# Kernel optimization log

Hardware: AMD Instinct MI355X
Metric: run time of the kernel (lower is better)

## Reference

```python
import jax, jax.numpy as jnp
import numpy as np


def conv1x1(x, w, b):
    # x: [B, Cin, D, H, W], w: [Cout, Cin], b: [Cout]
    return jnp.einsum('bcdhw,oc->bodhw', x, w) + b[None, :, None, None, None]


def setup_inputs() -> dict:
    key = jax.random.key(0)
    ks = jax.random.split(key, 9)
    B, C, D, H, W = 2, 64, 16, 16, 16
    Cc = 64          # context_dim
    C8 = C // 8      # inner attention dim
    s = 0.05
    return {
        'x': jax.random.normal(ks[0], (B, C, D, H, W), jnp.float32),
        'context': jax.random.normal(ks[1], (B, Cc, D, H, W), jnp.float32),
        'Wq': jax.random.normal(ks[2], (C8, C), jnp.float32) * s,
        'bq': jax.random.normal(ks[3], (C8,), jnp.float32) * s,
        'Wk': jax.random.normal(ks[4], (C8, Cc), jnp.float32) * s,
        'bk': jax.random.normal(ks[5], (C8,), jnp.float32) * s,
        'Wv': jax.random.normal(ks[6], (C, Cc), jnp.float32) * s,
        'bv': jax.random.normal(ks[7], (C,), jnp.float32) * s,
        'gamma': jax.random.normal(ks[8], (1,), jnp.float32) * s,
    }


def reference(x, context, Wq, bq, Wk, bk, Wv, bv, gamma):
    B, C, D, H, W = x.shape
    N = D * H * W
    q = conv1x1(x, Wq, bq).reshape(B, -1, N)        # [B, C/8, N]
    k = conv1x1(context, Wk, bk).reshape(B, -1, N)  # [B, C/8, N]
    v = conv1x1(context, Wv, bv).reshape(B, C, N)   # [B, C, N]
    # energy[b, n, m] = q[:, :, n] . k[:, :, m]  (no scaling, as in source)
    energy = jnp.einsum('bcn,bcm->bnm', q, k)       # [B, N, N]
    attn = jax.nn.softmax(energy, axis=-1)
    # out = v @ attn^T : out[b, c, n] = sum_m v[b, c, m] * attn[b, n, m]
    out = jnp.einsum('bcm,bnm->bcn', v, attn).reshape(B, C, D, H, W)
    return gamma[0] * out + x
```

## Files before the change

### kernel.cpp

```cpp
#include <hip/hip_runtime.h>

#define NTOK 4096

typedef __attribute__((ext_vector_type(8))) short short8;
typedef __attribute__((ext_vector_type(4))) float f32x4;
typedef __attribute__((ext_vector_type(4))) unsigned int uint4v;

__device__ __forceinline__ unsigned short f2bf(float f) {
    unsigned u = __float_as_uint(f);
    u += 0x7fffu + ((u >> 16) & 1u);
    return (unsigned short)(u >> 16);
}

__device__ __forceinline__ float bf2f(unsigned short h) {
    return __uint_as_float((unsigned)h << 16);
}

__device__ __forceinline__ unsigned int pk2(float lo, float hi) {
    return __builtin_amdgcn_perm(__float_as_uint(hi), __float_as_uint(lo), 0x07060302u);
}

__global__ __launch_bounds__(256) void proj(
    const float* __restrict__ x, const float* __restrict__ ctx,
    const float* __restrict__ Wq, const float* __restrict__ bq,
    const float* __restrict__ Wk, const float* __restrict__ bk,
    const float* __restrict__ Wv, const float* __restrict__ bv,
    unsigned short* __restrict__ qbf, unsigned short* __restrict__ kbf,
    unsigned short* __restrict__ vtp)
{
    __shared__ float sW[16 * 64];
    __shared__ float sB[16];
    int tid  = threadIdx.x;
    int ogrp = blockIdx.z;
    int b    = blockIdx.y;
    int n0   = blockIdx.x * 64;

    if (ogrp == 0) {
        for (int i = tid; i < 1024; i += 256)
            sW[i] = (i < 512) ? Wq[i] : Wk[i - 512];
        if (tid < 16) sB[tid] = (tid < 8) ? bq[tid] : bk[tid - 8];
    } else {
        for (int i = tid; i < 1024; i += 256)
            sW[i] = Wv[(ogrp - 1) * 1024 + i];
        if (tid < 16) sB[tid] = bv[(ogrp - 1) * 16 + tid];
    }
    __syncthreads();

    int nn   = tid & 63;
    int osub = tid >> 6;
    const float* inp = (ogrp == 0 && osub < 2) ? x : ctx;
    const float* ip  = inp + (size_t)b * 64 * NTOK + n0 + nn;

    float a0 = sB[osub * 4 + 0], a1 = sB[osub * 4 + 1];
    float a2 = sB[osub * 4 + 2], a3 = sB[osub * 4 + 3];
#pragma unroll 16
    for (int c = 0; c < 64; ++c) {
        float val = ip[(size_t)c * NTOK];
        a0 += sW[(osub * 4 + 0) * 64 + c] * val;
        a1 += sW[(osub * 4 + 1) * 64 + c] * val;
        a2 += sW[(osub * 4 + 2) * 64 + c] * val;
        a3 += sW[(osub * 4 + 3) * 64 + c] * val;
    }
    float av[4] = {a0, a1, a2, a3};

    if (ogrp == 0) {
        bool isq = osub < 2;
        float sc = isq ? 1.4426950408889634f : 1.0f;
        unsigned short* dst = isq ? qbf : kbf;
        int half = osub & 1;
        ushort4 pk = {f2bf(av[0] * sc), f2bf(av[1] * sc), f2bf(av[2] * sc), f2bf(av[3] * sc)};
        *(ushort4*)&dst[((size_t)b * NTOK + n0 + nn) * 8 + half * 4] = pk;
    } else {
        int cbase = (ogrp - 1) * 16 + osub * 4;
        int m   = n0 + nn;
        int T   = m >> 5;
        int mm  = m & 31;
        int p   = ((mm >> 2) & 3) * 8 + (mm >> 4) * 4 + (mm & 3);
        int qd  = p >> 3, j2 = p & 7;
        int ctv = cbase >> 4;
        unsigned short* vB = vtp + (size_t)b * 64 * NTOK
                           + ((size_t)T * 4 + ctv) * 512;
#pragma unroll
        for (int jj = 0; jj < 4; ++jj) {
            int lanev = ((cbase + jj) & 15) + 16 * qd;
            vB[lanev * 8 + j2] = f2bf(av[jj]);
        }
    }
}

__global__ __launch_bounds__(256, 2) void attn8(
    const unsigned short* __restrict__ qbf, const unsigned short* __restrict__ kbf,
    const unsigned short* __restrict__ vtp,
    unsigned short* __restrict__ partO, float* __restrict__ partL)
{
    __shared__ float sOc[4][16][68];
    __shared__ float sL[4][64];

    int tid  = threadIdx.x;
    int w    = tid >> 6, lane = tid & 63;
    int n    = lane & 15, quad = lane >> 4;
    int nt   = blockIdx.x;
    int b    = blockIdx.y;
    int qz   = blockIdx.z;
    int n0   = nt * 64;

    const f32x4 z4 = {0.f, 0.f, 0.f, 0.f};
    const short8 z8 = {0, 0, 0, 0, 0, 0, 0, 0};

    short8 bq[4];
#pragma unroll
    for (int g = 0; g < 4; ++g)
        bq[g] = (quad == 0)
            ? *(const short8*)&qbf[((size_t)b * NTOK + n0 + g * 16 + n) * 8]
            : z8;

    const unsigned short* kb = kbf + (size_t)b * NTOK * 8;
    const unsigned short* vb = vtp + (size_t)b * 64 * NTOK;
    int mwbase = qz * 512 + w * 128;

    f32x4 acc[4][4];
#pragma unroll
    for (int g = 0; g < 4; ++g)
#pragma unroll
        for (int ct = 0; ct < 4; ++ct) acc[g][ct] = z4;
    float lsum[4] = {0.f, 0.f, 0.f, 0.f};

    for (int h = 0; h < 2; ++h) {
        int m0 = mwbase + h * 64;
        int Tb = m0 >> 5;

        short8 kf0 = (quad == 0) ? *(const short8*)&kb[(size_t)(m0 + 0 * 16 + n) * 8] : z8;
        short8 kf1 = (quad == 0) ? *(const short8*)&kb[(size_t)(m0 + 1 * 16 + n) * 8] : z8;
        short8 kf2 = (quad == 0) ? *(const short8*)&kb[(size_t)(m0 + 2 * 16 + n) * 8] : z8;
        short8 kf3 = (quad == 0) ? *(const short8*)&kb[(size_t)(m0 + 3 * 16 + n) * 8] : z8;

        short8 af[2][4];
#pragma unroll
        for (int s = 0; s < 2; ++s)
#pragma unroll
            for (int ct = 0; ct < 4; ++ct)
                af[s][ct] = *(const short8*)&vb[(((size_t)(Tb + s) * 4 + ct) * 64 + lane) * 8];

#pragma unroll
        for (int g = 0; g < 4; ++g) {
            f32x4 sa0 = __builtin_amdgcn_mfma_f32_16x16x32_bf16(kf0, bq[g], z4, 0, 0, 0);
            f32x4 sa1 = __builtin_amdgcn_mfma_f32_16x16x32_bf16(kf1, bq[g], z4, 0, 0, 0);
            f32x4 sa2 = __builtin_amdgcn_mfma_f32_16x16x32_bf16(kf2, bq[g], z4, 0, 0, 0);
            f32x4 sa3 = __builtin_amdgcn_mfma_f32_16x16x32_bf16(kf3, bq[g], z4, 0, 0, 0);

            float e00 = __builtin_amdgcn_exp2f(sa0[0]), e01 = __builtin_amdgcn_exp2f(sa0[1]);
            float e02 = __builtin_amdgcn_exp2f(sa0[2]), e03 = __builtin_amdgcn_exp2f(sa0[3]);
            float e10 = __builtin_amdgcn_exp2f(sa1[0]), e11 = __builtin_amdgcn_exp2f(sa1[1]);
            float e12 = __builtin_amdgcn_exp2f(sa1[2]), e13 = __builtin_amdgcn_exp2f(sa1[3]);
            float e20 = __builtin_amdgcn_exp2f(sa2[0]), e21 = __builtin_amdgcn_exp2f(sa2[1]);
            float e22 = __builtin_amdgcn_exp2f(sa2[2]), e23 = __builtin_amdgcn_exp2f(sa2[3]);
            float e30 = __builtin_amdgcn_exp2f(sa3[0]), e31 = __builtin_amdgcn_exp2f(sa3[1]);
            float e32 = __builtin_amdgcn_exp2f(sa3[2]), e33 = __builtin_amdgcn_exp2f(sa3[3]);
            lsum[g] += ((e00 + e01) + (e02 + e03)) + ((e10 + e11) + (e12 + e13))
                     + ((e20 + e21) + (e22 + e23)) + ((e30 + e31) + (e32 + e33));

            uint4v t0, t1;
            t0[0] = pk2(e00, e01); t0[1] = pk2(e02, e03);
            t0[2] = pk2(e10, e11); t0[3] = pk2(e12, e13);
            t1[0] = pk2(e20, e21); t1[1] = pk2(e22, e23);
            t1[2] = pk2(e30, e31); t1[3] = pk2(e32, e33);
            short8 pf0 = __builtin_bit_cast(short8, t0);
            short8 pf1 = __builtin_bit_cast(short8, t1);

            acc[g][0] = __builtin_amdgcn_mfma_f32_16x16x32_bf16(af[0][0], pf0, acc[g][0], 0, 0, 0);
            acc[g][1] = __builtin_amdgcn_mfma_f32_16x16x32_bf16(af[0][1], pf0, acc[g][1], 0, 0, 0);
            acc[g][2] = __builtin_amdgcn_mfma_f32_16x16x32_bf16(af[0][2], pf0, acc[g][2], 0, 0, 0);
            acc[g][3] = __builtin_amdgcn_mfma_f32_16x16x32_bf16(af[0][3], pf0, acc[g][3], 0, 0, 0);
            acc[g][0] = __builtin_amdgcn_mfma_f32_16x16x32_bf16(af[1][0], pf1, acc[g][0], 0, 0, 0);
            acc[g][1] = __builtin_amdgcn_mfma_f32_16x16x32_bf16(af[1][1], pf1, acc[g][1], 0, 0, 0);
            acc[g][2] = __builtin_amdgcn_mfma_f32_16x16x32_bf16(af[1][2], pf1, acc[g][2], 0, 0, 0);
            acc[g][3] = __builtin_amdgcn_mfma_f32_16x16x32_bf16(af[1][3], pf1, acc[g][3], 0, 0, 0);
        }
    }

#pragma unroll
    for (int g = 0; g < 4; ++g) {
        float l = lsum[g];
        l += __shfl_xor(l, 16);
        l += __shfl_xor(l, 32);
        if (lane < 16) sL[w][g * 16 + n] = l;
    }

    unsigned short* pO = partO + ((size_t)((b * 64 + nt) * 8 + qz)) * 4096;
    float*          pL = partL + ((size_t)((b * 64 + nt) * 8 + qz)) * 64;

#pragma unroll
    for (int ct = 0; ct < 4; ++ct) {
        if (ct) __syncthreads();
#pragma unroll
        for (int g = 0; g < 4; ++g)
#pragma unroll
            for (int r = 0; r < 4; ++r)
                sOc[w][quad * 4 + r][g * 16 + n] = acc[g][ct][r];
        __syncthreads();
        for (int i = tid; i < 1024; i += 256) {
            int c16 = i >> 6, nn2 = i & 63;
            float s = sOc[0][c16][nn2] + sOc[1][c16][nn2]
                    + sOc[2][c16][nn2] + sOc[3][c16][nn2];
            pO[ct * 1024 + i] = f2bf(s);
        }
    }
    if (tid < 64)
        pL[tid] = sL[0][tid] + sL[1][tid] + sL[2][tid] + sL[3][tid];
}

__global__ __launch_bounds__(256) void mergeq(
    const unsigned short* __restrict__ partO, const float* __restrict__ partL,
    const float* __restrict__ x, const float* __restrict__ gamma,
    float* __restrict__ out)
{
    int tid = threadIdx.x;
    int nt  = blockIdx.x;
    int b   = blockIdx.y;
    int c   = tid >> 2;
    int j   = tid & 3;

    const unsigned short* pOb = partO + ((size_t)((b * 64 + nt) * 8)) * 4096;
    const float*          pLb = partL + ((size_t)((b * 64 + nt) * 8)) * 64;
    float g = gamma[0];
#pragma unroll
    for (int nq = 0; nq < 4; ++nq) {
        int ns = j * 16 + nq * 4;
        float4 o = {0.f, 0.f, 0.f, 0.f};
        float4 L = {0.f, 0.f, 0.f, 0.f};
#pragma unroll
        for (int qz = 0; qz < 8; ++qz) {
            ushort4 ov = *(const ushort4*)&pOb[qz * 4096 + c * 64 + ns];
            float4  lv = *(const float4*)&pLb[qz * 64 + ns];
            o.x += bf2f(ov.x); o.y += bf2f(ov.y);
            o.z += bf2f(ov.z); o.w += bf2f(ov.w);
            L.x += lv.x; L.y += lv.y; L.z += lv.z; L.w += lv.w;
        }
        size_t ob = ((size_t)b * 64 + c) * NTOK + nt * 64 + ns;
        float4 xv = *(const float4*)&x[ob];
        float4 res;
        res.x = g * (o.x / L.x) + xv.x;
        res.y = g * (o.y / L.y) + xv.y;
        res.z = g * (o.z / L.z) + xv.z;
        res.w = g * (o.w / L.w) + xv.w;
        *(float4*)&out[ob] = res;
    }
}

extern "C" void kernel_launch(void* const* d_in, const int* in_sizes, int n_in,
                              void* d_out, int out_size, void* d_ws, size_t ws_size,
                              hipStream_t stream) {
    const float* x     = (const float*)d_in[0];
    const float* ctx   = (const float*)d_in[1];
    const float* Wq    = (const float*)d_in[2];
    const float* bq    = (const float*)d_in[3];
    const float* Wk    = (const float*)d_in[4];
    const float* bk    = (const float*)d_in[5];
    const float* Wv    = (const float*)d_in[6];
    const float* bv    = (const float*)d_in[7];
    const float* gamma = (const float*)d_in[8];
    float* out = (float*)d_out;

    unsigned short* qbf   = (unsigned short*)d_ws;
    unsigned short* kbf   = qbf + 2 * NTOK * 8;
    unsigned short* vtp   = kbf + 2 * NTOK * 8;
    unsigned short* partO = vtp + 2 * 64 * NTOK;
    float*          partL = (float*)(partO + (size_t)2 * 64 * 8 * 4096);

    proj<<<dim3(64, 2, 5), 256, 0, stream>>>(x, ctx, Wq, bq, Wk, bk, Wv, bv, qbf, kbf, vtp);
    attn8<<<dim3(NTOK / 64, 2, 8), 256, 0, stream>>>(qbf, kbf, vtp, partO, partL);
    mergeq<<<dim3(NTOK / 64, 2), 256, 0, stream>>>(partO, partL, x, gamma, out);
}
```

Baseline: 97.33 us.

## Fuse split-K merge into attention kernel with 1024-thread blocks covering all keys

Replaces the 8-way split over key tokens plus a separate merge kernel with one 1024-thread block per 32 query tokens. Its 16 waves each cover 256 keys and reduce through shared memory before writing the normalized, gamma-scaled residual output directly. This removes the bf16 partial-output round trip through global memory and one kernel launch. In exchange there are fewer blocks (256), a larger 16-way LDS reduction, and uncoalesced scalar output writes. K/V reuse per block is also halved because each block now covers fewer queries.

```diff
diff --git a/kernel.cpp b/kernel.cpp
--- a/kernel.cpp
+++ b/kernel.cpp
@@ -10,10 +10,6 @@
     unsigned u = __float_as_uint(f);
     u += 0x7fffu + ((u >> 16) & 1u);
     return (unsigned short)(u >> 16);
-}
-
-__device__ __forceinline__ float bf2f(unsigned short h) {
-    return __uint_as_float((unsigned)h << 16);
 }
 
 __device__ __forceinline__ unsigned int pk2(float lo, float hi) {
@@ -88,44 +84,44 @@
     }
 }
 
-__global__ __launch_bounds__(256, 2) void attn8(
+__global__ __launch_bounds__(1024, 4) void attnf(
     const unsigned short* __restrict__ qbf, const unsigned short* __restrict__ kbf,
-    const unsigned short* __restrict__ vtp,
-    unsigned short* __restrict__ partO, float* __restrict__ partL)
+    const unsigned short* __restrict__ vtp, const float* __restrict__ x,
+    const float* __restrict__ gamma, float* __restrict__ out)
 {
-    __shared__ float sOc[4][16][68];
-    __shared__ float sL[4][64];
+    __shared__ float sOc[16][16][36];
+    __shared__ float sL[16][32];
+    __shared__ float sLt[32];
 
     int tid  = threadIdx.x;
     int w    = tid >> 6, lane = tid & 63;
     int n    = lane & 15, quad = lane >> 4;
     int nt   = blockIdx.x;
     int b    = blockIdx.y;
-    int qz   = blockIdx.z;
-    int n0   = nt * 64;
+    int n0   = nt * 32;
 
     const f32x4 z4 = {0.f, 0.f, 0.f, 0.f};
     const short8 z8 = {0, 0, 0, 0, 0, 0, 0, 0};
 
-    short8 bq[4];
-#pragma unroll
-    for (int g = 0; g < 4; ++g)
+    short8 bq[2];
+#pragma unroll
+    for (int g = 0; g < 2; ++g)
         bq[g] = (quad == 0)
             ? *(const short8*)&qbf[((size_t)b * NTOK + n0 + g * 16 + n) * 8]
             : z8;
 
     const unsigned short* kb = kbf + (size_t)b * NTOK * 8;
     const unsigned short* vb = vtp + (size_t)b * 64 * NTOK;
-    int mwbase = qz * 512 + w * 128;
-
-    f32x4 acc[4][4];
-#pragma unroll
-    for (int g = 0; g < 4; ++g)
+    int mwbase = w * 256;
+
+    f32x4 acc[2][4];
+#pragma unroll
+    for (int g = 0; g < 2; ++g)
 #pragma unroll
         for (int ct = 0; ct < 4; ++ct) acc[g][ct] = z4;
-    float lsum[4] = {0.f, 0.f, 0.f, 0.f};
-
-    for (int h = 0; h < 2; ++h) {
+    float lsum[2] = {0.f, 0.f};
+
+    for (int h = 0; h < 4; ++h) {
         int m0 = mwbase + h * 64;
         int Tb = m0 >> 5;
 
@@ -142,7 +138,7 @@
                 af[s][ct] = *(const short8*)&vb[(((size_t)(Tb + s) * 4 + ct) * 64 + lane) * 8];
 
 #pragma unroll
-        for (int g = 0; g < 4; ++g) {
+        for (int g = 0; g < 2; ++g) {
             f32x4 sa0 = __builtin_amdgcn_mfma_f32_16x16x32_bf16(kf0, bq[g], z4, 0, 0, 0);
             f32x4 sa1 = __builtin_amdgcn_mfma_f32_16x16x32_bf16(kf1, bq[g], z4, 0, 0, 0);
             f32x4 sa2 = __builtin_amdgcn_mfma_f32_16x16x32_bf16(kf2, bq[g], z4, 0, 0, 0);
@@ -179,71 +175,40 @@
     }
 
 #pragma unroll
-    for (int g = 0; g < 4; ++g) {
+    for (int g = 0; g < 2; ++g) {
         float l = lsum[g];
         l += __shfl_xor(l, 16);
         l += __shfl_xor(l, 32);
         if (lane < 16) sL[w][g * 16 + n] = l;
     }
-
-    unsigned short* pO = partO + ((size_t)((b * 64 + nt) * 8 + qz)) * 4096;
-    float*          pL = partL + ((size_t)((b * 64 + nt) * 8 + qz)) * 64;
-
+    __syncthreads();
+    if (tid < 32) {
+        float s = 0.f;
+#pragma unroll
+        for (int w2 = 0; w2 < 16; ++w2) s += sL[w2][tid];
+        sLt[tid] = s;
+    }
+    __syncthreads();
+
+    float gm = gamma[0];
 #pragma unroll
     for (int ct = 0; ct < 4; ++ct) {
         if (ct) __syncthreads();
 #pragma unroll
-        for (int g = 0; g < 4; ++g)
+        for (int g = 0; g < 2; ++g)
 #pragma unroll
             for (int r = 0; r < 4; ++r)
                 sOc[w][quad * 4 + r][g * 16 + n] = acc[g][ct][r];
         __syncthreads();
-        for (int i = tid; i < 1024; i += 256) {
-            int c16 = i >> 6, nn2 = i & 63;
-            float s = sOc[0][c16][nn2] + sOc[1][c16][nn2]
-                    + sOc[2][c16][nn2] + sOc[3][c16][nn2];
-            pO[ct * 1024 + i] = f2bf(s);
+        if (tid < 512) {
+            int c16 = tid >> 5, nn2 = tid & 31;
+            float s = 0.f;
+#pragma unroll
+            for (int w2 = 0; w2 < 16; ++w2) s += sOc[w2][c16][nn2];
+            int c = ct * 16 + c16;
+            size_t ob = ((size_t)b * 64 + c) * NTOK + n0 + nn2;
+            out[ob] = gm * (s / sLt[nn2]) + x[ob];
         }
-    }
-    if (tid < 64)
-        pL[tid] = sL[0][tid] + sL[1][tid] + sL[2][tid] + sL[3][tid];
-}
-
-__global__ __launch_bounds__(256) void mergeq(
-    const unsigned short* __restrict__ partO, const float* __restrict__ partL,
-    const float* __restrict__ x, const float* __restrict__ gamma,
-    float* __restrict__ out)
-{
-    int tid = threadIdx.x;
-    int nt  = blockIdx.x;
-    int b   = blockIdx.y;
-    int c   = tid >> 2;
-    int j   = tid & 3;
-
-    const unsigned short* pOb = partO + ((size_t)((b * 64 + nt) * 8)) * 4096;
-    const float*          pLb = partL + ((size_t)((b * 64 + nt) * 8)) * 64;
-    float g = gamma[0];
-#pragma unroll
-    for (int nq = 0; nq < 4; ++nq) {
-        int ns = j * 16 + nq * 4;
-        float4 o = {0.f, 0.f, 0.f, 0.f};
-        float4 L = {0.f, 0.f, 0.f, 0.f};
-#pragma unroll
-        for (int qz = 0; qz < 8; ++qz) {
-            ushort4 ov = *(const ushort4*)&pOb[qz * 4096 + c * 64 + ns];
-            float4  lv = *(const float4*)&pLb[qz * 64 + ns];
-            o.x += bf2f(ov.x); o.y += bf2f(ov.y);
-            o.z += bf2f(ov.z); o.w += bf2f(ov.w);
-            L.x += lv.x; L.y += lv.y; L.z += lv.z; L.w += lv.w;
-        }
-        size_t ob = ((size_t)b * 64 + c) * NTOK + nt * 64 + ns;
-        float4 xv = *(const float4*)&x[ob];
-        float4 res;
-        res.x = g * (o.x / L.x) + xv.x;
-        res.y = g * (o.y / L.y) + xv.y;
-        res.z = g * (o.z / L.z) + xv.z;
-        res.w = g * (o.w / L.w) + xv.w;
-        *(float4*)&out[ob] = res;
     }
 }
 
@@ -261,13 +226,10 @@
     const float* gamma = (const float*)d_in[8];
     float* out = (float*)d_out;
 
-    unsigned short* qbf   = (unsigned short*)d_ws;
-    unsigned short* kbf   = qbf + 2 * NTOK * 8;
-    unsigned short* vtp   = kbf + 2 * NTOK * 8;
-    unsigned short* partO = vtp + 2 * 64 * NTOK;
-    float*          partL = (float*)(partO + (size_t)2 * 64 * 8 * 4096);
+    unsigned short* qbf = (unsigned short*)d_ws;
+    unsigned short* kbf = qbf + 2 * NTOK * 8;
+    unsigned short* vtp = kbf + 2 * NTOK * 8;
 
     proj<<<dim3(64, 2, 5), 256, 0, stream>>>(x, ctx, Wq, bq, Wk, bk, Wv, bv, qbf, kbf, vtp);
-    attn8<<<dim3(NTOK / 64, 2, 8), 256, 0, stream>>>(qbf, kbf, vtp, partO, partL);
-    mergeq<<<dim3(NTOK / 64, 2), 256, 0, stream>>>(partO, partL, x, gamma, out);
-}
+    attnf<<<dim3(NTOK / 32, 2), 1024, 0, stream>>>(qbf, kbf, vtp, x, gamma, out);
+}
```

After: 108.3 us. 1.11x slower.
